# Kernel tuning notes

Hardware: AMD Instinct MI355X
Metric: run time of the kernel (lower is better)

Reference implementation:

```python
import jax, jax.numpy as jnp
import numpy as np
from jax import lax

N = 10000      # nodes (also LSTM seq_len, batch=1)
E = 640000     # edges
D = 256        # num_node_features
H = 512        # hidden_size (GIN out / LSTM input)
LH = 512       # lstm_hidden_size
BN_EPS = 1e-5


def setup_inputs() -> dict:
    key = jax.random.key(0)
    ks = jax.random.split(key, 20)
    def lin(k, out_d, in_d):
        s = 1.0 / np.sqrt(in_d)
        return jax.random.uniform(k, (out_d, in_d), jnp.float32, -s, s)
    def vec(k, d, fan):
        s = 1.0 / np.sqrt(fan)
        return jax.random.uniform(k, (d,), jnp.float32, -s, s)
    inp = {
        "x": jax.random.normal(ks[0], (N, D), jnp.float32),
        "edge_index": jax.random.randint(ks[1], (2, E), 0, N, jnp.int64),
        # GIN MLP: Linear(D,H) -> ReLU -> Linear(H,H)
        "w1": lin(ks[2], H, D), "b1": vec(ks[3], H, D),
        "w2": lin(ks[4], H, H), "b2": vec(ks[5], H, H),
        # BatchNorm1d(H) affine params (training-mode batch stats)
        "gamma": jnp.ones((H,), jnp.float32), "beta": jnp.zeros((H,), jnp.float32),
        # LSTM layer 0 (input H) and layer 1 (input LH); torch gate order i,f,g,o
        "w_ih0": lin(ks[6], 4 * LH, H), "w_hh0": lin(ks[7], 4 * LH, LH),
        "b_ih0": vec(ks[8], 4 * LH, LH), "b_hh0": vec(ks[9], 4 * LH, LH),
        "w_ih1": lin(ks[10], 4 * LH, LH), "w_hh1": lin(ks[11], 4 * LH, LH),
        "b_ih1": vec(ks[12], 4 * LH, LH), "b_hh1": vec(ks[13], 4 * LH, LH),
        # fc head
        "fc_w": lin(ks[14], 1, LH), "fc_b": vec(ks[15], 1, LH),
    }
    return inp


def _lstm_layer(xs, w_ih, w_hh, b_ih, b_hh):
    # xs: [T, in]; batch=1 squeezed. Precompute input projection as one big GEMM.
    Hh = w_hh.shape[1]
    pre = xs @ w_ih.T + b_ih + b_hh  # [T, 4H]
    def step(carry, p):
        h, c = carry
        gates = p + h @ w_hh.T
        i, f, g, o = jnp.split(gates, 4)
        i = jax.nn.sigmoid(i); f = jax.nn.sigmoid(f)
        g = jnp.tanh(g); o = jax.nn.sigmoid(o)
        c = f * c + i * g
        h = o * jnp.tanh(c)
        return (h, c), h
    init = (jnp.zeros((Hh,), xs.dtype), jnp.zeros((Hh,), xs.dtype))
    (h, c), hs = lax.scan(step, init, pre)
    return hs, h, c


def reference(x, edge_index, w1, b1, w2, b2, gamma, beta,
              w_ih0, w_hh0, b_ih0, b_hh0, w_ih1, w_hh1, b_ih1, b_hh1,
              fc_w, fc_b):
    n = x.shape[0]
    src, dst = edge_index[0], edge_index[1]
    # GINConv, eps=0: h_i = MLP(x_i + sum_{j->i} x_j)
    agg = jax.ops.segment_sum(x[src], dst, num_segments=n)
    h = x + agg
    h = jax.nn.relu(h @ w1.T + b1) @ w2.T + b2  # [N, H]
    # BatchNorm1d, training mode: biased batch stats over nodes
    mean = h.mean(axis=0)
    var = h.var(axis=0)
    h = (h - mean) * lax.rsqrt(var + BN_EPS) * gamma + beta
    h = jax.nn.relu(h)
    # dropout(p=0.5) treated as identity (eval mode, deterministic reference)
    # LSTM over the node sequence (batch=1), 2 stacked layers
    hs0, h0, c0 = _lstm_layer(h, w_ih0, w_hh0, b_ih0, b_hh0)
    hs1, h1, c1 = _lstm_layer(hs0, w_ih1, w_hh1, b_ih1, b_hh1)
    out = hs1 @ fc_w.T + fc_b          # [N, 1]
    out = out[:, 0][None, :]           # [1, N] after squeeze(2)
    h_n = jnp.stack([h0, h1])[:, None, :]  # [num_layers, 1, LH]
    c_n = jnp.stack([c0, c1])[:, None, :]
    return out, h_n, c_n
```

## Files before the change

kernel.cpp:

```cpp
#include <hip/hip_runtime.h>
#include <stdint.h>

#define N_NODES 10000
#define E_EDGES 640000
#define D_IN    256
#define H_DIM   512
#define K0      64
#define K1      128
#define RING    64

typedef unsigned short ushort_t;
typedef unsigned int   uint32;
typedef unsigned long long u64;

__device__ __forceinline__ float bf2f(ushort_t u) {
  union { uint32 i; float f; } v; v.i = ((uint32)u) << 16; return v.f;
}
__device__ __forceinline__ ushort_t f2bf(float f) {
  union { float f; uint32 i; } v; v.f = f;
  uint32 x = v.i;
  uint32 r = (x + 0x7FFFu + ((x >> 16) & 1u)) >> 16;
  return (ushort_t)r;
}

__device__ __forceinline__ float sigmoid_f(float x) {
  return 1.f / (1.f + __expf(-x));
}
__device__ __forceinline__ float tanh_f(float x) {
  x = fminf(10.f, fmaxf(-10.f, x));
  float e2 = __expf(2.f * x);
  return (e2 - 1.f) / (e2 + 1.f);
}

__device__ __forceinline__ u64 ld_c8(const u64* p) {
  return __hip_atomic_load(p, __ATOMIC_RELAXED, __HIP_MEMORY_SCOPE_AGENT);
}
__device__ __forceinline__ void st_c8(u64* p, float h, int flag) {
  u64 u = ((u64)(uint32)flag << 32) | (u64)__float_as_uint(h);
  __hip_atomic_store(p, u, __ATOMIC_RELAXED, __HIP_MEMORY_SCOPE_AGENT);
}
__device__ __forceinline__ void spin_relaxed(int* p, int target) {
  int guard = 0;
  while (__hip_atomic_load(p, __ATOMIC_RELAXED, __HIP_MEMORY_SCOPE_AGENT) < target) {
    __builtin_amdgcn_s_sleep(1);
    if (++guard > 100000000) break;
  }
  __atomic_signal_fence(__ATOMIC_ACQUIRE);
}

__global__ void k_zero(int* p) {
  p[blockIdx.x * 256 + threadIdx.x] = 0;
}

__global__ void k_detect(const int* eb, int* ctrl) {
  int v = eb[2 * (int)threadIdx.x + 1];
  if (v != 0) atomicOr(ctrl, 1);
}

__device__ __forceinline__ int edge_src(const int* eb, int flag, int e) {
  return flag ? eb[e] : eb[2 * e];
}
__device__ __forceinline__ int edge_dst(const int* eb, int flag, int e) {
  return flag ? eb[E_EDGES + e] : eb[2 * (E_EDGES + e)];
}

__global__ __launch_bounds__(256) void k_count(const int* eb, const int* ctrl, int* deg) {
  int e = blockIdx.x * 256 + threadIdx.x;
  if (e >= E_EDGES) return;
  int flag = ctrl[0];
  atomicAdd(&deg[edge_dst(eb, flag, e)], 1);
}

__global__ __launch_bounds__(1024) void k_prefix(const int* deg, int* off, int* cursor) {
  __shared__ int sums[1024];
  int tid = threadIdx.x;
  const int PER = 10;
  int base = tid * PER;
  int loc[PER];
  int s = 0;
  for (int i = 0; i < PER; i++) {
    int idx = base + i;
    int v = (idx < N_NODES) ? deg[idx] : 0;
    loc[i] = s; s += v;
  }
  sums[tid] = s;
  __syncthreads();
  for (int d = 1; d < 1024; d <<= 1) {
    int v = (tid >= d) ? sums[tid - d] : 0;
    __syncthreads();
    sums[tid] += v;
    __syncthreads();
  }
  int excl = (tid == 0) ? 0 : sums[tid - 1];
  for (int i = 0; i < PER; i++) {
    int idx = base + i;
    if (idx < N_NODES) { int o = excl + loc[i]; off[idx] = o; cursor[idx] = o; }
  }
  if (tid == 1023) off[N_NODES] = sums[1023];
}

__global__ __launch_bounds__(256) void k_fill(const int* eb, const int* ctrl, int* cursor, int* csr) {
  int e = blockIdx.x * 256 + threadIdx.x;
  if (e >= E_EDGES) return;
  int flag = ctrl[0];
  int d = edge_dst(eb, flag, e);
  int s = edge_src(eb, flag, e);
  int slot = atomicAdd(&cursor[d], 1);
  csr[slot] = s;
}

__global__ __launch_bounds__(256) void k_agg(const float* x, const int* off, const int* csr, float* h0) {
  int node = blockIdx.x;
  int f = threadIdx.x;
  float acc = x[(size_t)node * D_IN + f];
  int a = off[node], b = off[node + 1];
  for (int e = a; e < b; e++) {
    int s = csr[e];
    acc += x[(size_t)s * D_IN + f];
  }
  h0[(size_t)node * D_IN + f] = acc;
}

template<int KTOT, bool RELU, bool OUTBF16, bool TWOBIAS>
__global__ __launch_bounds__(256) void k_gemm(const float* __restrict__ A,
                                              const float* __restrict__ W,
                                              const float* __restrict__ bias1,
                                              const float* __restrict__ bias2,
                                              void* __restrict__ Cout, int M, int Ncols) {
  __shared__ float As[16][65];
  __shared__ float Ws[16][65];
  int tid = threadIdx.x;
  int tx = tid & 15, ty = tid >> 4;
  int by = blockIdx.x, bn = blockIdx.y;
  int lr  = tid >> 2;
  int lk4 = (tid & 3) * 4;
  float acc[4][4];
  #pragma unroll
  for (int i = 0; i < 4; i++)
    #pragma unroll
    for (int j = 0; j < 4; j++) acc[i][j] = 0.f;

  for (int k0 = 0; k0 < KTOT; k0 += 16) {
    int arow = by * 64 + lr;
    float4 av = make_float4(0.f, 0.f, 0.f, 0.f);
    if (arow < M) av = *(const float4*)(A + (size_t)arow * KTOT + k0 + lk4);
    As[lk4 + 0][lr] = av.x; As[lk4 + 1][lr] = av.y;
    As[lk4 + 2][lr] = av.z; As[lk4 + 3][lr] = av.w;
    float4 wv = *(const float4*)(W + (size_t)(bn * 64 + lr) * KTOT + k0 + lk4);
    Ws[lk4 + 0][lr] = wv.x; Ws[lk4 + 1][lr] = wv.y;
    Ws[lk4 + 2][lr] = wv.z; Ws[lk4 + 3][lr] = wv.w;
    __syncthreads();
    #pragma unroll
    for (int k = 0; k < 16; k++) {
      float a0 = As[k][ty], a1 = As[k][16 + ty], a2 = As[k][32 + ty], a3 = As[k][48 + ty];
      float w0 = Ws[k][tx], w1 = Ws[k][16 + tx], w2 = Ws[k][32 + tx], w3 = Ws[k][48 + tx];
      acc[0][0] += a0 * w0; acc[0][1] += a0 * w1; acc[0][2] += a0 * w2; acc[0][3] += a0 * w3;
      acc[1][0] += a1 * w0; acc[1][1] += a1 * w1; acc[1][2] += a1 * w2; acc[1][3] += a1 * w3;
      acc[2][0] += a2 * w0; acc[2][1] += a2 * w1; acc[2][2] += a2 * w2; acc[2][3] += a2 * w3;
      acc[3][0] += a3 * w0; acc[3][1] += a3 * w1; acc[3][2] += a3 * w2; acc[3][3] += a3 * w3;
    }
    __syncthreads();
  }
  float* Cf = (float*)Cout;
  ushort_t* Cb = (ushort_t*)Cout;
  #pragma unroll
  for (int i = 0; i < 4; i++) {
    int row = by * 64 + 16 * i + ty;
    if (row >= M) continue;
    #pragma unroll
    for (int j = 0; j < 4; j++) {
      int col = bn * 64 + 16 * j + tx;
      float b = bias1[col];
      if (TWOBIAS) b += bias2[col];
      float v = acc[i][j] + b;
      if (RELU) v = fmaxf(v, 0.f);
      if (OUTBF16) Cb[(size_t)row * Ncols + col] = f2bf(v);
      else         Cf[(size_t)row * Ncols + col] = v;
    }
  }
}

__global__ __launch_bounds__(256) void k_bnstats(const float* y2, float* colsum, float* colsumsq) {
  int b = blockIdx.x, tid = threadIdx.x;
  int r0 = b * 64, r1 = min(r0 + 64, N_NODES);
  float s0 = 0, q0 = 0, s1 = 0, q1 = 0;
  for (int r = r0; r < r1; r++) {
    float v0 = y2[(size_t)r * H_DIM + tid];
    float v1 = y2[(size_t)r * H_DIM + tid + 256];
    s0 += v0; q0 += v0 * v0; s1 += v1; q1 += v1 * v1;
  }
  atomicAdd(&colsum[tid], s0);        atomicAdd(&colsumsq[tid], q0);
  atomicAdd(&colsum[tid + 256], s1);  atomicAdd(&colsumsq[tid + 256], q1);
}

__global__ __launch_bounds__(256) void k_bnfin(float* colsum, float* colsumsq,
                                               const float* gamma, const float* beta) {
  int c = blockIdx.x * 256 + threadIdx.x;
  if (c >= H_DIM) return;
  float mean = colsum[c] * (1.f / N_NODES);
  float var  = colsumsq[c] * (1.f / N_NODES) - mean * mean;
  float sc = gamma[c] * rsqrtf(var + 1e-5f);
  float sh = beta[c] - mean * sc;
  colsum[c] = sc; colsumsq[c] = sh;
}

__global__ __launch_bounds__(256) void k_bnapply(float* y2, const float* sc, const float* sh) {
  size_t i = (size_t)blockIdx.x * 256 + threadIdx.x;
  int c = (int)(i & (H_DIM - 1));
  float v = y2[i] * sc[c] + sh[c];
  y2[i] = v > 0.f ? v : 0.f;
}

__global__ __launch_bounds__(256, 1) void k_lstm(const ushort_t* pre0, const float* w_hh0,
                                              const float* w_ih1, const float* w_hh1,
                                              const float* b_ih1, const float* b_hh1,
                                              u64* hs0c, u64* hs1c, float* hs1p,
                                              int* flags1, float* dout) {
  __shared__ float lds_in[2][512];
  __shared__ float lds_dots[32];
  __shared__ float lds_pre[2][32];
  int tid = threadIdx.x;
  int wave = tid >> 6, lane = tid & 63;
  int kp = lane & 7;
  int r = wave * 8 + (lane >> 3);
  int wg = blockIdx.x;

  float w_reg[64];
  float c_reg = 0.f;

  if (wg < K0) {
    int u0 = wg * 8;
    {
      int grow = (r >> 3) * H_DIM + u0 + (r & 7);
      const float* src = w_hh0 + (size_t)grow * H_DIM + kp * 64;
      #pragma unroll
      for (int i = 0; i < 16; i++) {
        int j0 = ((i + 2 * kp) & 15) * 4;
        float4 v = *(const float4*)(src + j0);
        w_reg[4 * i + 0] = v.x; w_reg[4 * i + 1] = v.y;
        w_reg[4 * i + 2] = v.z; w_reg[4 * i + 3] = v.w;
      }
    }
    float pf = 0.f;
    if (tid < 32)
      pf = bf2f(pre0[(tid >> 3) * H_DIM + u0 + (tid & 7)]);

    for (int t = 0; t < N_NODES; t++) {
      int phase = t & 1;
      if (t > 0) {
        const u64* pa = hs0c + ((t - 1) & (RING - 1)) * 512 + tid;
        const u64* pb = pa + 256;
        u64 ua, ub; int guard = 0;
        for (;;) {
          ua = ld_c8(pa); ub = ld_c8(pb);
          if (((int)(ua >> 32) == t && (int)(ub >> 32) == t) || ++guard > 100000000) break;
        }
        lds_in[0][tid]       = __uint_as_float((uint32)ua);
        lds_in[0][tid + 256] = __uint_as_float((uint32)ub);
      }
      if (tid < 32) lds_pre[phase][tid] = pf;
      __syncthreads();
      if (tid < 32 && t + 1 < N_NODES)
        pf = bf2f(pre0[(size_t)(t + 1) * 2048 + (tid >> 3) * H_DIM + u0 + (tid & 7)]);
      if ((t & 31) == 0 && t >= RING && tid < K1)
        spin_relaxed(&flags1[tid * 16], t - 32);
      if (t > 0) {
        const float* hrow = &lds_in[0][kp * 64];
        float dot = 0.f;
        #pragma unroll
        for (int i = 0; i < 16; i++) {
          int j0 = ((i + 2 * kp) & 15) * 4;
          float4 h4 = *(const float4*)(hrow + j0);
          dot += w_reg[4 * i] * h4.x + w_reg[4 * i + 1] * h4.y
               + w_reg[4 * i + 2] * h4.z + w_reg[4 * i + 3] * h4.w;
        }
        dot += __shfl_xor(dot, 1, 64);
        dot += __shfl_xor(dot, 2, 64);
        dot += __shfl_xor(dot, 4, 64);
        if (kp == 0) lds_dots[r] = dot;
      } else if (tid < 32) {
        lds_dots[tid] = 0.f;
      }
      __syncthreads();
      if (wave == 0) {
        float val = 0.f;
        if (lane < 32) {
          float pre = lds_dots[lane] + lds_pre[phase][lane];
          val = ((lane >> 3) == 2) ? tanh_f(pre) : sigmoid_f(pre);
        }
        int j = lane & 7;
        float ii = __shfl(val, j, 64);
        float ff = __shfl(val, 8 + j, 64);
        float gg = __shfl(val, 16 + j, 64);
        float oo = __shfl(val, 24 + j, 64);
        if (lane < 8) {
          c_reg = ff * c_reg + ii * gg;
          float hv = oo * tanh_f(c_reg);
          st_c8(hs0c + (t & (RING - 1)) * 512 + u0 + lane, hv, t + 1);
          if (t == N_NODES - 1) {
            dout[10000 + u0 + lane] = hv;
            dout[11024 + u0 + lane] = c_reg;
          }
        }
      }
    }
  } else {
    int wg1 = wg - K0;
    int u0 = wg1 * 4;
    int m = r >> 4;
    {
      int gj = r & 15;
      int grow = (gj >> 2) * H_DIM + u0 + (gj & 3);
      const float* src = (m ? w_hh1 : w_ih1) + (size_t)grow * H_DIM + kp * 64;
      #pragma unroll
      for (int i = 0; i < 16; i++) {
        int j0 = ((i + 2 * kp) & 15) * 4;
        float4 v = *(const float4*)(src + j0);
        w_reg[4 * i + 0] = v.x; w_reg[4 * i + 1] = v.y;
        w_reg[4 * i + 2] = v.z; w_reg[4 * i + 3] = v.w;
      }
    }
    if (tid < 16) {
      int g = tid >> 2, j = tid & 3;
      int grow = g * H_DIM + u0 + j;
      lds_pre[0][tid] = b_ih1[grow] + b_hh1[grow];
    }
    __syncthreads();

    for (int s = 0; s < N_NODES; s++) {
      {
        bool need1 = (s > 0);
        const u64* p0a = hs0c + (s & (RING - 1)) * 512 + tid;
        const u64* p0b = p0a + 256;
        const u64* p1a = hs1c + ((s - 1) & (RING - 1)) * 512 + tid;
        const u64* p1b = p1a + 256;
        u64 u0a, u0b, u1a, u1b; int guard = 0;
        for (;;) {
          u0a = ld_c8(p0a); u0b = ld_c8(p0b);
          u1a = ld_c8(p1a); u1b = ld_c8(p1b);
          bool ok0 = ((int)(u0a >> 32) == s + 1) && ((int)(u0b >> 32) == s + 1);
          bool ok1 = !need1 || (((int)(u1a >> 32) == s) && ((int)(u1b >> 32) == s));
          if ((ok0 && ok1) || ++guard > 100000000) break;
        }
        if (!need1) { u1a = 0; u1b = 0; }
        lds_in[0][tid]       = __uint_as_float((uint32)u0a);
        lds_in[0][tid + 256] = __uint_as_float((uint32)u0b);
        lds_in[1][tid]       = __uint_as_float((uint32)u1a);
        lds_in[1][tid + 256] = __uint_as_float((uint32)u1b);
      }
      __syncthreads();
      if (tid == 0)
        __hip_atomic_store(&flags1[wg1 * 16], s + 1, __ATOMIC_RELAXED, __HIP_MEMORY_SCOPE_AGENT);
      {
        const float* hrow = &lds_in[m][kp * 64];
        float dot = 0.f;
        #pragma unroll
        for (int i = 0; i < 16; i++) {
          int j0 = ((i + 2 * kp) & 15) * 4;
          float4 h4 = *(const float4*)(hrow + j0);
          dot += w_reg[4 * i] * h4.x + w_reg[4 * i + 1] * h4.y
               + w_reg[4 * i + 2] * h4.z + w_reg[4 * i + 3] * h4.w;
        }
        dot += __shfl_xor(dot, 1, 64);
        dot += __shfl_xor(dot, 2, 64);
        dot += __shfl_xor(dot, 4, 64);
        if (kp == 0) lds_dots[r] = dot;
      }
      __syncthreads();
      if (wave == 0) {
        float val = 0.f;
        if (lane < 16) {
          float pre = lds_dots[lane] + lds_dots[16 + lane] + lds_pre[0][lane];
          val = ((lane >> 2) == 2) ? tanh_f(pre) : sigmoid_f(pre);
        }
        int j = lane & 3;
        float ii = __shfl(val, j, 64);
        float ff = __shfl(val, 4 + j, 64);
        float gg = __shfl(val, 8 + j, 64);
        float oo = __shfl(val, 12 + j, 64);
        if (lane < 4) {
          c_reg = ff * c_reg + ii * gg;
          float hv = oo * tanh_f(c_reg);
          st_c8(hs1c + (s & (RING - 1)) * 512 + u0 + lane, hv, s + 1);
          hs1p[(size_t)s * H_DIM + u0 + lane] = hv;
          if (s == N_NODES - 1) {
            dout[10512 + u0 + lane] = hv;
            dout[11536 + u0 + lane] = c_reg;
          }
        }
      }
    }
  }
}

__global__ __launch_bounds__(256) void k_fc(const float* hs1, const float* fc_w,
                                            const float* fc_b, float* dout) {
  int row = blockIdx.x * 4 + (threadIdx.x >> 6);
  int lane = threadIdx.x & 63;
  float acc = 0.f;
  #pragma unroll
  for (int j = 0; j < 8; j++) {
    int c = lane + 64 * j;
    acc += hs1[(size_t)row * H_DIM + c] * fc_w[c];
  }
  for (int d = 32; d; d >>= 1) acc += __shfl_xor(acc, d, 64);
  if (lane == 0) dout[row] = acc + fc_b[0];
}

extern "C" void kernel_launch(void* const* d_in, const int* in_sizes, int n_in,
                              void* d_out, int out_size, void* d_ws, size_t ws_size,
                              hipStream_t stream) {
  const float* x     = (const float*)d_in[0];
  const int*   eb    = (const int*)d_in[1];
  const float* w1    = (const float*)d_in[2];
  const float* b1    = (const float*)d_in[3];
  const float* w2    = (const float*)d_in[4];
  const float* b2    = (const float*)d_in[5];
  const float* gamma = (const float*)d_in[6];
  const float* beta  = (const float*)d_in[7];
  const float* w_ih0 = (const float*)d_in[8];
  const float* w_hh0 = (const float*)d_in[9];
  const float* b_ih0 = (const float*)d_in[10];
  const float* b_hh0 = (const float*)d_in[11];
  const float* w_ih1 = (const float*)d_in[12];
  const float* w_hh1 = (const float*)d_in[13];
  const float* b_ih1 = (const float*)d_in[14];
  const float* b_hh1 = (const float*)d_in[15];
  const float* fc_w  = (const float*)d_in[16];
  const float* fc_b  = (const float*)d_in[17];
  float* dout = (float*)d_out;
  char* ws = (char*)d_ws;

  int*    ctrl     = (int*)(ws + 0);
  int*    flags1   = (int*)(ws + 256);
  float*  colsum   = (float*)(ws + 8448);
  float*  colsumsq = (float*)(ws + 10496);
  int*    deg      = (int*)(ws + 12544);
  u64*    hs0c     = (u64*)(ws + 57344);
  u64*    hs1c     = (u64*)(ws + 319488);
  float*  y1       = (float*)(ws + 581632);
  float*  y2       = (float*)(ws + 21061632);
  float*  h0       = y2;
  ushort_t* pre0   = (ushort_t*)(ws + 41541632);
  int*    off      = (int*)(ws + 41541632);
  int*    cursor   = (int*)(ws + 41582080);
  int*    csr      = (int*)(ws + 41622528);
  float*  hs1p     = y1;

  k_zero<<<56, 256, 0, stream>>>((int*)ws);
  k_detect<<<1, 64, 0, stream>>>(eb, ctrl);
  k_count<<<2500, 256, 0, stream>>>(eb, ctrl, deg);
  k_prefix<<<1, 1024, 0, stream>>>(deg, off, cursor);
  k_fill<<<2500, 256, 0, stream>>>(eb, ctrl, cursor, csr);
  k_agg<<<10000, 256, 0, stream>>>(x, off, csr, h0);

  dim3 g1(157, 8);
  k_gemm<256, true,  false, false><<<g1, 256, 0, stream>>>(h0, w1, b1, nullptr, y1, N_NODES, 512);
  dim3 g2(157, 8);
  k_gemm<512, false, false, false><<<g2, 256, 0, stream>>>(y1, w2, b2, nullptr, y2, N_NODES, 512);

  k_bnstats<<<157, 256, 0, stream>>>(y2, colsum, colsumsq);
  k_bnfin<<<2, 256, 0, stream>>>(colsum, colsumsq, gamma, beta);
  k_bnapply<<<20000, 256, 0, stream>>>(y2, colsum, colsumsq);

  dim3 g3(157, 32);
  k_gemm<512, false, true, true><<<g3, 256, 0, stream>>>(y2, w_ih0, b_ih0, b_hh0, pre0, N_NODES, 2048);

  k_lstm<<<192, 256, 0, stream>>>(pre0, w_hh0, w_ih1, w_hh1, b_ih1, b_hh1,
                                  hs0c, hs1c, hs1p, flags1, dout);
  k_fc<<<2500, 256, 0, stream>>>(hs1p, fc_w, fc_b, dout);
}
```

Measured before the change: 26.20 ms.

## Fuse both LSTM layers into each workgroup with wavefront-skewed timesteps

```diff
diff --git a/kernel.cpp b/kernel.cpp
--- a/kernel.cpp
+++ b/kernel.cpp
@@ -5,8 +5,7 @@
 #define E_EDGES 640000
 #define D_IN    256
 #define H_DIM   512
-#define K0      64
-#define K1      128
+#define KWG     64
 #define RING    64
 
 typedef unsigned short ushort_t;
@@ -38,14 +37,6 @@
 __device__ __forceinline__ void st_c8(u64* p, float h, int flag) {
   u64 u = ((u64)(uint32)flag << 32) | (u64)__float_as_uint(h);
   __hip_atomic_store(p, u, __ATOMIC_RELAXED, __HIP_MEMORY_SCOPE_AGENT);
-}
-__device__ __forceinline__ void spin_relaxed(int* p, int target) {
-  int guard = 0;
-  while (__hip_atomic_load(p, __ATOMIC_RELAXED, __HIP_MEMORY_SCOPE_AGENT) < target) {
-    __builtin_amdgcn_s_sleep(1);
-    if (++guard > 100000000) break;
-  }
-  __atomic_signal_fence(__ATOMIC_ACQUIRE);
 }
 
 __global__ void k_zero(int* p) {
@@ -214,78 +205,115 @@
 __global__ __launch_bounds__(256, 1) void k_lstm(const ushort_t* pre0, const float* w_hh0,
                                               const float* w_ih1, const float* w_hh1,
                                               const float* b_ih1, const float* b_hh1,
-                                              u64* hs0c, u64* hs1c, float* hs1p,
-                                              int* flags1, float* dout) {
-  __shared__ float lds_in[2][512];
-  __shared__ float lds_dots[32];
+                                              u64* hs0c, u64* hs1c, float* hs1p, float* dout) {
+  __shared__ float lds_h[2][1024];
+  __shared__ float lds_d0[32], lds_d1[32];
   __shared__ float lds_pre[2][32];
   int tid = threadIdx.x;
   int wave = tid >> 6, lane = tid & 63;
   int kp = lane & 7;
   int r = wave * 8 + (lane >> 3);
   int wg = blockIdx.x;
-
-  float w_reg[64];
+  int u0 = wg * 8;
+
+  float w0r[64], w1r[128];
+  {
+    int grow = (r >> 3) * H_DIM + u0 + (r & 7);
+    const float* src = w_hh0 + (size_t)grow * H_DIM + kp * 64;
+    #pragma unroll
+    for (int i = 0; i < 16; i++) {
+      int j0 = ((i + 2 * kp) & 15) * 4;
+      float4 v = *(const float4*)(src + j0);
+      w0r[4*i+0]=v.x; w0r[4*i+1]=v.y; w0r[4*i+2]=v.z; w0r[4*i+3]=v.w;
+    }
+  }
+  {
+    int grow = (r >> 3) * H_DIM + u0 + (r & 7);
+    const float* src = (kp < 4) ? (w_ih1 + (size_t)grow * H_DIM + kp * 128)
+                                : (w_hh1 + (size_t)grow * H_DIM + (kp - 4) * 128);
+    #pragma unroll
+    for (int i = 0; i < 32; i++) {
+      int j0 = ((i + 5 * kp) & 31) * 4;
+      float4 v = *(const float4*)(src + j0);
+      w1r[4*i+0]=v.x; w1r[4*i+1]=v.y; w1r[4*i+2]=v.z; w1r[4*i+3]=v.w;
+    }
+  }
+  float bias1 = 0.f;
+  if (wave == 1 && lane < 32) {
+    int grow = (lane >> 3) * H_DIM + u0 + (lane & 7);
+    bias1 = b_ih1[grow] + b_hh1[grow];
+  }
+  float pf = 0.f;
+  if (tid < 32)
+    pf = bf2f(pre0[(tid >> 3) * H_DIM + u0 + (tid & 7)]);
   float c_reg = 0.f;
 
-  if (wg < K0) {
-    int u0 = wg * 8;
-    {
-      int grow = (r >> 3) * H_DIM + u0 + (r & 7);
-      const float* src = w_hh0 + (size_t)grow * H_DIM + kp * 64;
-      #pragma unroll
-      for (int i = 0; i < 16; i++) {
-        int j0 = ((i + 2 * kp) & 15) * 4;
-        float4 v = *(const float4*)(src + j0);
-        w_reg[4 * i + 0] = v.x; w_reg[4 * i + 1] = v.y;
-        w_reg[4 * i + 2] = v.z; w_reg[4 * i + 3] = v.w;
+  for (int t = 0; t <= N_NODES; t++) {
+    int p = t & 1;
+    if (t > 0) {
+      int slot0 = (t - 1) & (RING - 1);
+      int slot1 = (t - 2) & (RING - 1);
+      const u64* a0 = hs0c + (size_t)slot0 * 512 + tid;
+      const u64* b0 = a0 + 256;
+      const u64* a1 = hs1c + (size_t)slot1 * 512 + tid;
+      const u64* b1 = a1 + 256;
+      bool need1 = (t >= 2);
+      u64 ua, ub, va = 0, vb = 0; int guard = 0;
+      for (;;) {
+        ua = ld_c8(a0); ub = ld_c8(b0);
+        bool ok = ((int)(ua >> 32) == t) && ((int)(ub >> 32) == t);
+        if (need1) {
+          va = ld_c8(a1); vb = ld_c8(b1);
+          ok = ok && ((int)(va >> 32) == t - 1) && ((int)(vb >> 32) == t - 1);
+        }
+        if (ok || ++guard > 50000000) break;
       }
-    }
-    float pf = 0.f;
-    if (tid < 32)
-      pf = bf2f(pre0[(tid >> 3) * H_DIM + u0 + (tid & 7)]);
-
-    for (int t = 0; t < N_NODES; t++) {
-      int phase = t & 1;
-      if (t > 0) {
-        const u64* pa = hs0c + ((t - 1) & (RING - 1)) * 512 + tid;
-        const u64* pb = pa + 256;
-        u64 ua, ub; int guard = 0;
-        for (;;) {
-          ua = ld_c8(pa); ub = ld_c8(pb);
-          if (((int)(ua >> 32) == t && (int)(ub >> 32) == t) || ++guard > 100000000) break;
-        }
-        lds_in[0][tid]       = __uint_as_float((uint32)ua);
-        lds_in[0][tid + 256] = __uint_as_float((uint32)ub);
-      }
-      if (tid < 32) lds_pre[phase][tid] = pf;
-      __syncthreads();
-      if (tid < 32 && t + 1 < N_NODES)
-        pf = bf2f(pre0[(size_t)(t + 1) * 2048 + (tid >> 3) * H_DIM + u0 + (tid & 7)]);
-      if ((t & 31) == 0 && t >= RING && tid < K1)
-        spin_relaxed(&flags1[tid * 16], t - 32);
-      if (t > 0) {
-        const float* hrow = &lds_in[0][kp * 64];
-        float dot = 0.f;
+      if (!need1) { va = 0; vb = 0; }
+      lds_h[p][tid]        = __uint_as_float((uint32)ua);
+      lds_h[p][tid + 256]  = __uint_as_float((uint32)ub);
+      lds_h[p][512 + tid]  = __uint_as_float((uint32)va);
+      lds_h[p][768 + tid]  = __uint_as_float((uint32)vb);
+    }
+    if (tid < 32 && t < N_NODES) lds_pre[p][tid] = pf;
+    __syncthreads();
+    if (tid < 32 && t + 1 < N_NODES)
+      pf = bf2f(pre0[(size_t)(t + 1) * 2048 + (tid >> 3) * H_DIM + u0 + (tid & 7)]);
+    if (t > 0) {
+      if (t < N_NODES) {
+        const float* h = &lds_h[p][kp * 64];
+        float d = 0.f;
         #pragma unroll
         for (int i = 0; i < 16; i++) {
           int j0 = ((i + 2 * kp) & 15) * 4;
-          float4 h4 = *(const float4*)(hrow + j0);
-          dot += w_reg[4 * i] * h4.x + w_reg[4 * i + 1] * h4.y
-               + w_reg[4 * i + 2] * h4.z + w_reg[4 * i + 3] * h4.w;
-        }
-        dot += __shfl_xor(dot, 1, 64);
-        dot += __shfl_xor(dot, 2, 64);
-        dot += __shfl_xor(dot, 4, 64);
-        if (kp == 0) lds_dots[r] = dot;
-      } else if (tid < 32) {
-        lds_dots[tid] = 0.f;
+          float4 x = *(const float4*)(h + j0);
+          d += w0r[4*i]*x.x + w0r[4*i+1]*x.y + w0r[4*i+2]*x.z + w0r[4*i+3]*x.w;
+        }
+        d += __shfl_xor(d, 1, 64);
+        d += __shfl_xor(d, 2, 64);
+        d += __shfl_xor(d, 4, 64);
+        if (kp == 0) lds_d0[r] = d;
       }
-      __syncthreads();
-      if (wave == 0) {
+      {
+        const float* h = &lds_h[p][kp * 128];
+        float d = 0.f;
+        #pragma unroll
+        for (int i = 0; i < 32; i++) {
+          int j0 = ((i + 5 * kp) & 31) * 4;
+          float4 x = *(const float4*)(h + j0);
+          d += w1r[4*i]*x.x + w1r[4*i+1]*x.y + w1r[4*i+2]*x.z + w1r[4*i+3]*x.w;
+        }
+        d += __shfl_xor(d, 1, 64);
+        d += __shfl_xor(d, 2, 64);
+        d += __shfl_xor(d, 4, 64);
+        if (kp == 0) lds_d1[r] = d;
+      }
+    }
+    __syncthreads();
+    if (wave == 0) {
+      if (t < N_NODES) {
         float val = 0.f;
         if (lane < 32) {
-          float pre = lds_dots[lane] + lds_pre[phase][lane];
+          float pre = (t > 0 ? lds_d0[lane] : 0.f) + lds_pre[p][lane];
           val = ((lane >> 3) == 2) ? tanh_f(pre) : sigmoid_f(pre);
         }
         int j = lane & 7;
@@ -296,92 +324,30 @@
         if (lane < 8) {
           c_reg = ff * c_reg + ii * gg;
           float hv = oo * tanh_f(c_reg);
-          st_c8(hs0c + (t & (RING - 1)) * 512 + u0 + lane, hv, t + 1);
+          st_c8(hs0c + (size_t)(t & (RING - 1)) * 512 + u0 + lane, hv, t + 1);
           if (t == N_NODES - 1) {
             dout[10000 + u0 + lane] = hv;
             dout[11024 + u0 + lane] = c_reg;
           }
         }
       }
-    }
-  } else {
-    int wg1 = wg - K0;
-    int u0 = wg1 * 4;
-    int m = r >> 4;
-    {
-      int gj = r & 15;
-      int grow = (gj >> 2) * H_DIM + u0 + (gj & 3);
-      const float* src = (m ? w_hh1 : w_ih1) + (size_t)grow * H_DIM + kp * 64;
-      #pragma unroll
-      for (int i = 0; i < 16; i++) {
-        int j0 = ((i + 2 * kp) & 15) * 4;
-        float4 v = *(const float4*)(src + j0);
-        w_reg[4 * i + 0] = v.x; w_reg[4 * i + 1] = v.y;
-        w_reg[4 * i + 2] = v.z; w_reg[4 * i + 3] = v.w;
-      }
-    }
-    if (tid < 16) {
-      int g = tid >> 2, j = tid & 3;
-      int grow = g * H_DIM + u0 + j;
-      lds_pre[0][tid] = b_ih1[grow] + b_hh1[grow];
-    }
-    __syncthreads();
-
-    for (int s = 0; s < N_NODES; s++) {
-      {
-        bool need1 = (s > 0);
-        const u64* p0a = hs0c + (s & (RING - 1)) * 512 + tid;
-        const u64* p0b = p0a + 256;
-        const u64* p1a = hs1c + ((s - 1) & (RING - 1)) * 512 + tid;
-        const u64* p1b = p1a + 256;
-        u64 u0a, u0b, u1a, u1b; int guard = 0;
-        for (;;) {
-          u0a = ld_c8(p0a); u0b = ld_c8(p0b);
-          u1a = ld_c8(p1a); u1b = ld_c8(p1b);
-          bool ok0 = ((int)(u0a >> 32) == s + 1) && ((int)(u0b >> 32) == s + 1);
-          bool ok1 = !need1 || (((int)(u1a >> 32) == s) && ((int)(u1b >> 32) == s));
-          if ((ok0 && ok1) || ++guard > 100000000) break;
-        }
-        if (!need1) { u1a = 0; u1b = 0; }
-        lds_in[0][tid]       = __uint_as_float((uint32)u0a);
-        lds_in[0][tid + 256] = __uint_as_float((uint32)u0b);
-        lds_in[1][tid]       = __uint_as_float((uint32)u1a);
-        lds_in[1][tid + 256] = __uint_as_float((uint32)u1b);
-      }
-      __syncthreads();
-      if (tid == 0)
-        __hip_atomic_store(&flags1[wg1 * 16], s + 1, __ATOMIC_RELAXED, __HIP_MEMORY_SCOPE_AGENT);
-      {
-        const float* hrow = &lds_in[m][kp * 64];
-        float dot = 0.f;
-        #pragma unroll
-        for (int i = 0; i < 16; i++) {
-          int j0 = ((i + 2 * kp) & 15) * 4;
-          float4 h4 = *(const float4*)(hrow + j0);
-          dot += w_reg[4 * i] * h4.x + w_reg[4 * i + 1] * h4.y
-               + w_reg[4 * i + 2] * h4.z + w_reg[4 * i + 3] * h4.w;
-        }
-        dot += __shfl_xor(dot, 1, 64);
-        dot += __shfl_xor(dot, 2, 64);
-        dot += __shfl_xor(dot, 4, 64);
-        if (kp == 0) lds_dots[r] = dot;
-      }
-      __syncthreads();
-      if (wave == 0) {
+    } else if (wave == 1) {
+      if (t >= 1) {
+        int s = t - 1;
         float val = 0.f;
-        if (lane < 16) {
-          float pre = lds_dots[lane] + lds_dots[16 + lane] + lds_pre[0][lane];
-          val = ((lane >> 2) == 2) ? tanh_f(pre) : sigmoid_f(pre);
-        }
-        int j = lane & 3;
+        if (lane < 32) {
+          float pre = lds_d1[lane] + bias1;
+          val = ((lane >> 3) == 2) ? tanh_f(pre) : sigmoid_f(pre);
+        }
+        int j = lane & 7;
         float ii = __shfl(val, j, 64);
-        float ff = __shfl(val, 4 + j, 64);
-        float gg = __shfl(val, 8 + j, 64);
-        float oo = __shfl(val, 12 + j, 64);
-        if (lane < 4) {
+        float ff = __shfl(val, 8 + j, 64);
+        float gg = __shfl(val, 16 + j, 64);
+        float oo = __shfl(val, 24 + j, 64);
+        if (lane < 8) {
           c_reg = ff * c_reg + ii * gg;
           float hv = oo * tanh_f(c_reg);
-          st_c8(hs1c + (s & (RING - 1)) * 512 + u0 + lane, hv, s + 1);
+          st_c8(hs1c + (size_t)(s & (RING - 1)) * 512 + u0 + lane, hv, s + 1);
           hs1p[(size_t)s * H_DIM + u0 + lane] = hv;
           if (s == N_NODES - 1) {
             dout[10512 + u0 + lane] = hv;
@@ -432,19 +398,18 @@
   char* ws = (char*)d_ws;
 
   int*    ctrl     = (int*)(ws + 0);
-  int*    flags1   = (int*)(ws + 256);
-  float*  colsum   = (float*)(ws + 8448);
-  float*  colsumsq = (float*)(ws + 10496);
-  int*    deg      = (int*)(ws + 12544);
-  u64*    hs0c     = (u64*)(ws + 57344);
-  u64*    hs1c     = (u64*)(ws + 319488);
-  float*  y1       = (float*)(ws + 581632);
-  float*  y2       = (float*)(ws + 21061632);
+  float*  colsum   = (float*)(ws + 4096);
+  float*  colsumsq = (float*)(ws + 6144);
+  int*    deg      = (int*)(ws + 8192);
+  u64*    hs0c     = (u64*)(ws + 65536);
+  u64*    hs1c     = (u64*)(ws + 327680);
+  float*  y1       = (float*)(ws + 589824);
+  float*  y2       = (float*)(ws + 21069824);
   float*  h0       = y2;
-  ushort_t* pre0   = (ushort_t*)(ws + 41541632);
-  int*    off      = (int*)(ws + 41541632);
-  int*    cursor   = (int*)(ws + 41582080);
-  int*    csr      = (int*)(ws + 41622528);
+  ushort_t* pre0   = (ushort_t*)(ws + 41549824);
+  int*    off      = (int*)(ws + 41549824);
+  int*    cursor   = (int*)(ws + 41589828);
+  int*    csr      = (int*)(ws + 41629828);
   float*  hs1p     = y1;
 
   k_zero<<<56, 256, 0, stream>>>((int*)ws);
@@ -466,7 +431,7 @@
   dim3 g3(157, 32);
   k_gemm<512, false, true, true><<<g3, 256, 0, stream>>>(y2, w_ih0, b_ih0, b_hh0, pre0, N_NODES, 2048);
 
-  k_lstm<<<192, 256, 0, stream>>>(pre0, w_hh0, w_ih1, w_hh1, b_ih1, b_hh1,
-                                  hs0c, hs1c, hs1p, flags1, dout);
+  k_lstm<<<KWG, 256, 0, stream>>>(pre0, w_hh0, w_ih1, w_hh1, b_ih1, b_hh1,
+                                  hs0c, hs1c, hs1p, dout);
   k_fc<<<2500, 256, 0, stream>>>(hs1p, fc_w, fc_b, dout);
 }
```

Measured after the change: 40.93 ms. 1.56x slower.
